# Performance work log

Measured on AMD Instinct MI355X. Metric: run time of the kernel, lower is better.

Reference implementation:

```python
import jax, jax.numpy as jnp
import numpy as np

T, D, H, HD = 2048, 2048, 16, 128
ROPE_BASE = 10000.0
NEG = jnp.float32(-1e30)


def rms_norm(x):
    # F.rms_norm(x, (x.size(-1),)) with default eps = dtype eps
    eps = jnp.finfo(x.dtype).eps
    return x * jax.lax.rsqrt(jnp.mean(x * x, axis=-1, keepdims=True) + eps)


def rotary(x):
    # x: [1, T, H, hd]; half-split rotation as in Rotary.forward
    hd = x.shape[-1]
    inv_freq = (1.0 / ROPE_BASE) ** (jnp.arange(0, hd, 2, dtype=jnp.float32) / hd)
    t = jnp.arange(x.shape[1], dtype=jnp.float32)
    freqs = jnp.outer(t, inv_freq)                      # [T, hd/2]
    cos = jnp.cos(freqs)[None, :, None, :]
    sin = jnp.sin(freqs)[None, :, None, :]
    x1, x2 = jnp.split(x, 2, axis=-1)
    return jnp.concatenate([x1 * cos + x2 * sin, -x1 * sin + x2 * cos], axis=-1)


def setup_inputs() -> dict:
    key = jax.random.key(0)
    ks = jax.random.split(key, 10)
    w = lambda k, shape: jax.random.normal(k, shape, jnp.float32) * 0.02
    return {
        "x":  jax.random.normal(ks[0], (1, T, D), jnp.float32),
        "vi": jax.random.normal(ks[1], (1, T, H, HD), jnp.float32),
        "x0": jax.random.normal(ks[2], (1, T, D), jnp.float32),
        "wq": w(ks[3], (D, D)),
        "wk": w(ks[4], (D, D)),
        "wv": w(ks[5], (D, D)),
        "wo": w(ks[6], (D, D)),
        "lamb": jnp.float32(0.5),
        "lambdas": jnp.array([1.0, 0.0], jnp.float32),
        "w_fc": w(ks[7], (4 * D, D)),
        "w_proj": w(ks[8], (D, 4 * D)),
    }


def reference(x, vi, x0, wq, wk, wv, wo, lamb, lambdas, w_fc, w_proj):
    # Block: residual blend with initial embedding x0
    xb = lambdas[0] * x + lambdas[1] * x0
    xn = rms_norm(xb)

    # --- CausalSelfAttention ---
    q = (xn @ wq.T).reshape(1, T, H, HD)
    k = (xn @ wk.T).reshape(1, T, H, HD)
    v = (xn @ wv.T).reshape(1, T, H, HD)
    v = (1.0 - lamb) * v + lamb * vi                     # value-embedding blend
    q = rotary(rms_norm(q))
    k = rotary(rms_norm(k))

    scale = 1.0 / jnp.sqrt(jnp.float32(HD))              # flex_attention default scale
    scores = jnp.einsum('bqhd,bkhd->bhqk', q, k) * scale # [1,H,T,T]
    causal = jnp.tril(jnp.ones((T, T), bool))
    scores = jnp.where(causal[None, None], scores, NEG)
    attn = jax.nn.softmax(scores, axis=-1)
    y = jnp.einsum('bhqk,bkhd->bqhd', attn, v).reshape(1, T, D)
    a = y @ wo.T                                         # attention output REPLACES x (no residual)

    # --- MLP with squared ReLU ---
    h = rms_norm(a) @ w_fc.T
    h = jnp.square(jax.nn.relu(h))
    out = a + h @ w_proj.T
    return out
```

## Files before the change

### kernel.cpp

```cpp
#include <hip/hip_runtime.h>
#include <hip/hip_bf16.h>

typedef __bf16 bf16;
typedef __bf16 bf16x8 __attribute__((ext_vector_type(8)));
typedef float f32x4 __attribute__((ext_vector_type(4)));
typedef unsigned int u32x4 __attribute__((ext_vector_type(4)));

#define DD 2048
#define DD2 4194304ull
#define G10_LDS 65536

__device__ __forceinline__ void glds16(const void* g, void* l) {
  __builtin_amdgcn_global_load_lds((const __attribute__((address_space(1))) void*)g,
                                   (__attribute__((address_space(3))) void*)l, 16, 0, 0);
}

__device__ __forceinline__ f32x4 mfma16(bf16x8 a, bf16x8 b, f32x4 c) {
  return __builtin_amdgcn_mfma_f32_16x16x32_bf16(a, b, c, 0, 0, 0);
}

__device__ __forceinline__ unsigned pk2(float lo, float hi) {
  unsigned short a = __builtin_bit_cast(unsigned short, (bf16)lo);
  unsigned short b = __builtin_bit_cast(unsigned short, (bf16)hi);
  return (unsigned)a | ((unsigned)b << 16);
}

__global__ __launch_bounds__(256) void cvt_seg(const float* __restrict__ s0, const float* __restrict__ s1,
                                               const float* __restrict__ s2, const float* __restrict__ s3,
                                               bf16* __restrict__ dst, int seglog, size_t total) {
  size_t i = ((size_t)blockIdx.x * 256 + threadIdx.x) * 16;
  const size_t stride = (size_t)gridDim.x * 256 * 16;
  for (; i < total; i += stride) {
    int seg = (int)(i >> seglog);
    const float* src = (seg == 0) ? s0 : (seg == 1) ? s1 : (seg == 2) ? s2 : s3;
    size_t loc = i - ((size_t)seg << seglog);
    float4 a0 = *(const float4*)(src + loc);
    float4 a1 = *(const float4*)(src + loc + 4);
    float4 a2 = *(const float4*)(src + loc + 8);
    float4 a3 = *(const float4*)(src + loc + 12);
    bf16x8 o0, o1;
    o0[0] = (bf16)a0.x; o0[1] = (bf16)a0.y; o0[2] = (bf16)a0.z; o0[3] = (bf16)a0.w;
    o0[4] = (bf16)a1.x; o0[5] = (bf16)a1.y; o0[6] = (bf16)a1.z; o0[7] = (bf16)a1.w;
    o1[0] = (bf16)a2.x; o1[1] = (bf16)a2.y; o1[2] = (bf16)a2.z; o1[3] = (bf16)a2.w;
    o1[4] = (bf16)a3.x; o1[5] = (bf16)a3.y; o1[6] = (bf16)a3.z; o1[7] = (bf16)a3.w;
    *(bf16x8*)(dst + i) = o0;
    *(bf16x8*)(dst + i + 8) = o1;
  }
}

template<bool BLEND>
__global__ __launch_bounds__(256) void prenorm_k(const float* __restrict__ x, const float* __restrict__ x0,
                                                 const float* __restrict__ lambdas, bf16* __restrict__ out) {
  const int t = blockIdx.x, tid = threadIdx.x;
  const float4* xr = (const float4*)(x + (size_t)t * DD);
  float4 a0 = xr[2 * tid], a1 = xr[2 * tid + 1];
  float v[8] = {a0.x, a0.y, a0.z, a0.w, a1.x, a1.y, a1.z, a1.w};
  if (BLEND) {
    const float l0 = lambdas[0], l1 = lambdas[1];
    const float4* yr = (const float4*)(x0 + (size_t)t * DD);
    float4 b0 = yr[2 * tid], b1 = yr[2 * tid + 1];
    float w[8] = {b0.x, b0.y, b0.z, b0.w, b1.x, b1.y, b1.z, b1.w};
#pragma unroll
    for (int i = 0; i < 8; ++i) v[i] = l0 * v[i] + l1 * w[i];
  }
  float ss = 0.f;
#pragma unroll
  for (int i = 0; i < 8; ++i) ss += v[i] * v[i];
#pragma unroll
  for (int off = 1; off < 64; off <<= 1) ss += __shfl_xor(ss, off, 64);
  __shared__ float red[4];
  const int wid = tid >> 6;
  if ((tid & 63) == 0) red[wid] = ss;
  __syncthreads();
  ss = red[0] + red[1] + red[2] + red[3];
  const float sc = rsqrtf(ss * (1.0f / DD) + 1.1920928955078125e-07f);
  bf16x8 o;
#pragma unroll
  for (int i = 0; i < 8; ++i) o[i] = (bf16)(v[i] * sc);
  *(bf16x8*)(out + (size_t)t * DD + tid * 8) = o;
}

__global__ __launch_bounds__(256) void rope_k(bf16* __restrict__ qg, bf16* __restrict__ kg) {
  const int tid = threadIdx.x, lane = tid & 63, wid = tid >> 6;
  const int p = blockIdx.x * 4 + wid;
  bf16* base = ((p >> 15) ? kg : qg);
  const int t = (p >> 4) & 2047, hh = p & 15;
  base += (size_t)t * DD + hh * 128;
  float x1 = (float)base[lane], x2 = (float)base[lane + 64];
  float ss = x1 * x1 + x2 * x2;
#pragma unroll
  for (int off = 1; off < 64; off <<= 1) ss += __shfl_xor(ss, off, 64);
  const float sc = rsqrtf(ss * (1.0f / 128.0f) + 1.1920928955078125e-07f);
  x1 *= sc; x2 *= sc;
  const float fr = (float)t * exp2f((float)lane * (-13.287712379549449f / 64.0f));
  const float s = sinf(fr), c = cosf(fr);
  base[lane]      = (bf16)(x1 * c + x2 * s);
  base[lane + 64] = (bf16)(-x1 * s + x2 * c);
}

__global__ __launch_bounds__(256) void vt_k(const bf16* __restrict__ v, bf16* __restrict__ vt) {
  __shared__ alignas(16) bf16 tile[16 * 128];
  const int tb = blockIdx.x, hb = blockIdx.y, tid = threadIdx.x;
  glds16(v + (size_t)(tb * 16 + (tid >> 4)) * DD + hb * 128 + (tid & 15) * 8, tile + tid * 8);
  __syncthreads();
  const int d_l = tid & 127, tc = tid >> 7;
  bf16x8 o;
#pragma unroll
  for (int i = 0; i < 8; ++i) o[i] = tile[(tc * 8 + i) * 128 + d_l];
  *(bf16x8*)(vt + (size_t)(hb * 128 + d_l) * DD + tb * 16 + tc * 8) = o;
}

__device__ __forceinline__ void g10_stageA(const bf16* A, int Kstride, int row0, int k0,
                                           bf16* buf, int hm, int tid) {
  int prl = tid >> 3, slot = tid & 7;
  int wmb = prl >> 5, r31 = prl & 31;
  glds16(A + (size_t)(row0 + wmb * 64 + hm * 32 + r31) * Kstride + k0 + ((slot ^ (prl & 7)) * 8),
         buf + hm * 4096 + tid * 8);
}
__device__ __forceinline__ void g10_stageB(const bf16* B, int Kstride, int col0, int k0,
                                           bf16* buf, int hn, int tid) {
  int pbl = tid >> 3, slot = tid & 7;
  int wnb = pbl >> 4, c15 = pbl & 15;
  glds16(B + (size_t)(col0 + wnb * 32 + hn * 16 + c15) * Kstride + k0 + ((slot ^ (pbl & 7)) * 8),
         buf + 8192 + hn * 4096 + tid * 8);
}

__device__ __forceinline__ void gemm10_core(const bf16* __restrict__ A, const bf16* __restrict__ B,
                                            int Kstride, int Klen, int row0, int col0,
                                            bf16* smem, f32x4 (&acc)[4][2]) {
  const int tid = threadIdx.x, lane = tid & 63, wid = tid >> 6;
  const int wm = wid >> 2, wn = wid & 3;
  const int l15 = lane & 15, g = lane >> 4;
  const int NT = Klen >> 6;
  g10_stageA(A, Kstride, row0, 0, smem, 0, tid);
  g10_stageB(B, Kstride, col0, 0, smem, 0, tid);
  g10_stageB(B, Kstride, col0, 0, smem, 1, tid);
  g10_stageA(A, Kstride, row0, 0, smem, 1, tid);
  asm volatile("s_waitcnt vmcnt(2)" ::: "memory");
  __builtin_amdgcn_s_barrier();

  bf16x8 a[2][2], b0[2], b1[2];
  for (int t = 0; t < NT; ++t) {
    bf16* cb = smem + (t & 1) * 16384;
    bf16* nb = smem + ((t + 1) & 1) * 16384;
    const int kst = (t + 1) << 6;
    const bool st = (t + 1) < NT;
#pragma unroll
    for (int mm = 0; mm < 2; ++mm)
#pragma unroll
      for (int ks = 0; ks < 2; ++ks) {
        int pr = wm * 32 + mm * 16 + l15;
        a[mm][ks] = *(const bf16x8*)(cb + pr * 64 + (((ks * 4 + g) ^ (pr & 7)) * 8));
      }
#pragma unroll
    for (int ks = 0; ks < 2; ++ks) {
      int pb = wn * 16 + l15;
      b0[ks] = *(const bf16x8*)(cb + 8192 + pb * 64 + (((ks * 4 + g) ^ (pb & 7)) * 8));
    }
    if (st) { g10_stageA(A, Kstride, row0, kst, nb, 0, tid);
              asm volatile("s_waitcnt vmcnt(2)" ::: "memory"); }
    else    { asm volatile("s_waitcnt vmcnt(1)" ::: "memory"); }
    __builtin_amdgcn_s_barrier();
    __builtin_amdgcn_s_setprio(1);
#pragma unroll
    for (int mm = 0; mm < 2; ++mm)
#pragma unroll
      for (int ks = 0; ks < 2; ++ks)
        acc[mm][0] = mfma16(a[mm][ks], b0[ks], acc[mm][0]);
    __builtin_amdgcn_s_setprio(0);
#pragma unroll
    for (int ks = 0; ks < 2; ++ks) {
      int pb = wn * 16 + l15;
      b1[ks] = *(const bf16x8*)(cb + 8192 + 4096 + pb * 64 + (((ks * 4 + g) ^ (pb & 7)) * 8));
    }
    if (st) { g10_stageB(B, Kstride, col0, kst, nb, 0, tid);
              asm volatile("s_waitcnt vmcnt(2)" ::: "memory"); }
    else    { asm volatile("s_waitcnt vmcnt(0)" ::: "memory"); }
    __builtin_amdgcn_s_barrier();
    __builtin_amdgcn_s_setprio(1);
#pragma unroll
    for (int mm = 0; mm < 2; ++mm)
#pragma unroll
      for (int ks = 0; ks < 2; ++ks)
        acc[mm][1] = mfma16(a[mm][ks], b1[ks], acc[mm][1]);
    __builtin_amdgcn_s_setprio(0);
#pragma unroll
    for (int mm = 0; mm < 2; ++mm)
#pragma unroll
      for (int ks = 0; ks < 2; ++ks) {
        int pr = 64 + wm * 32 + mm * 16 + l15;
        a[mm][ks] = *(const bf16x8*)(cb + pr * 64 + (((ks * 4 + g) ^ (pr & 7)) * 8));
      }
    if (st) g10_stageB(B, Kstride, col0, kst, nb, 1, tid);
    __builtin_amdgcn_s_barrier();
    __builtin_amdgcn_s_setprio(1);
#pragma unroll
    for (int mm = 0; mm < 2; ++mm)
#pragma unroll
      for (int ks = 0; ks < 2; ++ks)
        acc[2 + mm][0] = mfma16(a[mm][ks], b0[ks], acc[2 + mm][0]);
    __builtin_amdgcn_s_setprio(0);
    if (st) { g10_stageA(A, Kstride, row0, kst, nb, 1, tid);
              asm volatile("s_waitcnt vmcnt(2)" ::: "memory"); }
    __builtin_amdgcn_s_barrier();
    __builtin_amdgcn_s_setprio(1);
#pragma unroll
    for (int mm = 0; mm < 2; ++mm)
#pragma unroll
      for (int ks = 0; ks < 2; ++ks)
        acc[2 + mm][1] = mfma16(a[mm][ks], b1[ks], acc[2 + mm][1]);
    __builtin_amdgcn_s_setprio(0);
  }
}

#define GEMM10_EPI(STMT)                                                       \
  { const int lane_ = threadIdx.x & 63, wid_ = threadIdx.x >> 6;               \
    const int l15_ = lane_ & 15, g_ = lane_ >> 4;                              \
    const int wm_ = wid_ >> 2, wn_ = wid_ & 3;                                 \
    _Pragma("unroll") for (int m = 0; m < 4; ++m)                              \
    _Pragma("unroll") for (int n = 0; n < 2; ++n)                              \
    _Pragma("unroll") for (int j = 0; j < 4; ++j) {                            \
      int grow = row0 + wm_ * 64 + (m >> 1) * 32 + (m & 1) * 16 + g_ * 4 + j;  \
      int gcol = col0 + wn_ * 32 + n * 16 + l15_;                              \
      float vacc = acc[m][n][j];                                               \
      STMT; } }

__global__ __launch_bounds__(512, 4) void gemm10_qkv(const bf16* __restrict__ A,
    const bf16* __restrict__ Wq, const bf16* __restrict__ Wk, const bf16* __restrict__ Wv,
    bf16* __restrict__ oq, bf16* __restrict__ ok, bf16* __restrict__ ov,
    const float* __restrict__ vi, const float* __restrict__ lambp) {
  extern __shared__ bf16 smem10[];
  const int z = blockIdx.z;
  const bf16* B = (z == 0) ? Wq : (z == 1) ? Wk : Wv;
  bf16* out = (z == 0) ? oq : (z == 1) ? ok : ov;
  const int row0 = blockIdx.y * 128, col0 = blockIdx.x * 128;
  f32x4 acc[4][2] = {};
  gemm10_core(A, B, DD, DD, row0, col0, smem10, acc);
  if (z < 2) {
    GEMM10_EPI( out[(size_t)grow * DD + gcol] = (bf16)vacc; )
  } else {
    const float lam = *lambp;
    GEMM10_EPI( out[(size_t)grow * DD + gcol] =
                  (bf16)((1.0f - lam) * vacc + lam * vi[(size_t)grow * DD + gcol]); )
  }
}

__global__ __launch_bounds__(512, 4) void gemm10_part(const bf16* __restrict__ A, const bf16* __restrict__ B,
                                                      float* __restrict__ o1, int N, int Kstride, int Klen) {
  extern __shared__ bf16 smem10[];
  const int row0 = blockIdx.y * 128, col0 = blockIdx.x * 128;
  const int kofs = blockIdx.z * Klen;
  float* out = o1 + (size_t)blockIdx.z * DD2;
  f32x4 acc[4][2] = {};
  gemm10_core(A + kofs, B + kofs, Kstride, Klen, row0, col0, smem10, acc);
  GEMM10_EPI( out[(size_t)grow * N + gcol] = vacc; )
}

__global__ __launch_bounds__(512, 4) void gemm10_relu(const bf16* __restrict__ A, const bf16* __restrict__ B,
                                                      bf16* __restrict__ out, int N, int Kstride, int Klen) {
  extern __shared__ bf16 smem10[];
  const int row0 = blockIdx.y * 128, col0 = blockIdx.x * 128;
  f32x4 acc[4][2] = {};
  gemm10_core(A, B, Kstride, Klen, row0, col0, smem10, acc);
  GEMM10_EPI( float r = fmaxf(vacc, 0.f); out[(size_t)grow * N + gcol] = (bf16)(r * r); )
}

__global__ __launch_bounds__(256) void wo_red_prenorm(const float* __restrict__ pa,
                                                      float* __restrict__ a_f, bf16* __restrict__ an) {
  const int t = blockIdx.x, tid = threadIdx.x;
  const size_t base = (size_t)t * DD + tid * 8;
  float v[8];
#pragma unroll
  for (int h = 0; h < 2; ++h) {
    size_t i = base + h * 4;
    float4 r0 = *(const float4*)(pa + i);
    float4 r1 = *(const float4*)(pa + DD2 + i);
    v[h*4+0] = r0.x + r1.x;
    v[h*4+1] = r0.y + r1.y;
    v[h*4+2] = r0.z + r1.z;
    v[h*4+3] = r0.w + r1.w;
  }
  *(float4*)(a_f + base)     = make_float4(v[0], v[1], v[2], v[3]);
  *(float4*)(a_f + base + 4) = make_float4(v[4], v[5], v[6], v[7]);
  float ss = 0.f;
#pragma unroll
  for (int i = 0; i < 8; ++i) ss += v[i] * v[i];
#pragma unroll
  for (int off = 1; off < 64; off <<= 1) ss += __shfl_xor(ss, off, 64);
  __shared__ float red[4];
  if ((tid & 63) == 0) red[tid >> 6] = ss;
  __syncthreads();
  ss = red[0] + red[1] + red[2] + red[3];
  const float sc = rsqrtf(ss * (1.0f / DD) + 1.1920928955078125e-07f);
  bf16x8 o;
#pragma unroll
  for (int i = 0; i < 8; ++i) o[i] = (bf16)(v[i] * sc);
  *(bf16x8*)(an + base) = o;
}

__global__ __launch_bounds__(256) void proj_red(const float* __restrict__ pa,
                                                const float* __restrict__ a_f, float* __restrict__ out) {
  const size_t base = ((size_t)blockIdx.x * 256 + threadIdx.x) * 8;
#pragma unroll
  for (int h = 0; h < 2; ++h) {
    size_t i = base + h * 4;
    float4 r = *(const float4*)(a_f + i);
    float4 u = *(const float4*)(pa + i);
    float4 w = *(const float4*)(pa + DD2 + i);
    *(float4*)(out + i) = make_float4(r.x + u.x + w.x, r.y + u.y + w.y,
                                      r.z + u.z + w.z, r.w + u.w + w.w);
  }
}

__device__ __forceinline__ void att_stageK(const bf16* kg, int h, int kt, bf16* dst, int tid) {
#pragma unroll
  for (int r = 0; r < 2; ++r) {
    int e = tid + r * 256, row = e >> 4, slot = e & 15;
    glds16(kg + (size_t)(kt * 32 + row) * DD + h * 128 + ((slot ^ (row & 7)) * 8), dst + e * 8);
  }
}
__device__ __forceinline__ void att_stageV(const bf16* vtg, int h, int kt, bf16* dst, int tid) {
#pragma unroll
  for (int r = 0; r < 2; ++r) {
    int e = tid + r * 256, d = e >> 2, slot = e & 3;
    glds16(vtg + (size_t)(h * 128 + d) * DD + kt * 32 + ((slot ^ ((d >> 1) & 3)) * 8), dst + e * 8);
  }
}

__global__ __launch_bounds__(256) void attn_k(const bf16* __restrict__ qg, const bf16* __restrict__ kg,
                                              const bf16* __restrict__ vtg, bf16* __restrict__ yg) {
  __shared__ alignas(16) bf16 Ks[3][32 * 128];
  __shared__ alignas(16) bf16 Vt[3][128 * 32];
  const int h = blockIdx.y, qb = 31 - blockIdx.x;
  const int tid = threadIdx.x, lane = tid & 63, wid = tid >> 6;
  const int l15 = lane & 15, g = lane >> 4, swl = l15 & 7;
  const int qrow = qb * 64 + wid * 16;
  const float scale = 0.08838834764831845f;
  bf16x8 aQ[4];
  {
    const bf16* qp = qg + (size_t)(qrow + l15) * DD + h * 128 + g * 8;
#pragma unroll
    for (int kc = 0; kc < 4; ++kc) aQ[kc] = *(const bf16x8*)(qp + kc * 32);
  }
  f32x4 acc[8] = {};
  float lsum = 0.f;
  const int nkt = qb * 2 + 2;
  att_stageK(kg, h, 0, Ks[0], tid);
  att_stageV(vtg, h, 0, Vt[0], tid);
  att_stageK(kg, h, 1, Ks[1], tid);
  att_stageV(vtg, h, 1, Vt[1], tid);
  asm volatile("s_waitcnt vmcnt(4)" ::: "memory");
  __builtin_amdgcn_s_barrier();
  int cur = 0;
  for (int kt = 0; kt < nkt; ++kt) {
    const int kbase = kt * 32;
    const int nb = (cur >= 1) ? cur - 1 : 2;
    bf16x8 kf0[4], kf1[4];
#pragma unroll
    for (int kc = 0; kc < 4; ++kc) {
      kf0[kc] = *(const bf16x8*)(Ks[cur] + l15 * 128 + (((kc * 4 + g) ^ swl) * 8));
      kf1[kc] = *(const bf16x8*)(Ks[cur] + (16 + l15) * 128 + (((kc * 4 + g) ^ swl) * 8));
    }
    if (kt + 2 < nkt) { att_stageK(kg, h, kt + 2, Ks[nb], tid);
                        att_stageV(vtg, h, kt + 2, Vt[nb], tid); }
    f32x4 S0 = {}, S1 = {};
#pragma unroll
    for (int kc = 0; kc < 4; ++kc) {
      S0 = mfma16(kf0[kc], aQ[kc], S0);
      S1 = mfma16(kf1[kc], aQ[kc], S1);
    }
    const int q = qrow + l15;
    float p0[4], p1[4];
#pragma unroll
    for (int j = 0; j < 4; ++j) {
      int k0 = kbase + 4 * g + j;
      p0[j] = (k0 <= q) ? __expf(S0[j] * scale) : 0.f;
      p1[j] = (k0 + 16 <= q) ? __expf(S1[j] * scale) : 0.f;
      lsum += p0[j] + p1[j];
    }
    unsigned w0 = pk2(p0[0], p0[1]), w1 = pk2(p0[2], p0[3]);
    unsigned w2 = pk2(p1[0], p1[1]), w3 = pk2(p1[2], p1[3]);
    const int s0l = (g & 1) * 32 + l15, s1l = s0l + 16;
    const bool hi = g >= 2;
    unsigned t00 = __shfl(w0, s0l, 64), t10 = __shfl(w1, s0l, 64);
    unsigned t01 = __shfl(w0, s1l, 64), t11 = __shfl(w1, s1l, 64);
    unsigned u00 = __shfl(w2, s0l, 64), u10 = __shfl(w3, s0l, 64);
    unsigned u01 = __shfl(w2, s1l, 64), u11 = __shfl(w3, s1l, 64);
    u32x4 av = { hi ? u00 : t00, hi ? u10 : t10, hi ? u01 : t01, hi ? u11 : t11 };
    bf16x8 aP = __builtin_bit_cast(bf16x8, av);
#pragma unroll
    for (int dt = 0; dt < 8; ++dt) {
      int d = dt * 16 + l15;
      bf16x8 bV = *(const bf16x8*)(Vt[cur] + d * 32 + ((g ^ ((d >> 1) & 3)) * 8));
      acc[dt] = mfma16(aP, bV, acc[dt]);
    }
    if (kt + 1 < nkt) {
      if (kt + 2 < nkt) { asm volatile("s_waitcnt vmcnt(4)" ::: "memory"); }
      else              { asm volatile("s_waitcnt vmcnt(0)" ::: "memory"); }
      __builtin_amdgcn_s_barrier();
    }
    cur = (cur == 2) ? 0 : cur + 1;
  }
  lsum += __shfl_xor(lsum, 16, 64);
  lsum += __shfl_xor(lsum, 32, 64);
  f32x4 linv;
#pragma unroll
  for (int j = 0; j < 4; ++j) linv[j] = 1.0f / __shfl(lsum, 4 * g + j, 64);
#pragma unroll
  for (int dt = 0; dt < 8; ++dt)
#pragma unroll
    for (int j = 0; j < 4; ++j) {
      int q = qrow + 4 * g + j;
      yg[(size_t)q * DD + h * 128 + dt * 16 + l15] = (bf16)(acc[dt][j] * linv[j]);
    }
}

extern "C" void kernel_launch(void* const* d_in, const int* in_sizes, int n_in,
                              void* d_out, int out_size, void* d_ws, size_t ws_size,
                              hipStream_t stream) {
  const float* x       = (const float*)d_in[0];
  const float* vi      = (const float*)d_in[1];
  const float* x0      = (const float*)d_in[2];
  const float* wq      = (const float*)d_in[3];
  const float* wk      = (const float*)d_in[4];
  const float* wv      = (const float*)d_in[5];
  const float* wo      = (const float*)d_in[6];
  const float* lamb    = (const float*)d_in[7];
  const float* lambdas = (const float*)d_in[8];
  const float* wfc     = (const float*)d_in[9];
  const float* wproj   = (const float*)d_in[10];
  float* out = (float*)d_out;

  (void)hipFuncSetAttribute(reinterpret_cast<const void*>(gemm10_qkv),
                            hipFuncAttributeMaxDynamicSharedMemorySize, G10_LDS);
  (void)hipFuncSetAttribute(reinterpret_cast<const void*>(gemm10_part),
                            hipFuncAttributeMaxDynamicSharedMemorySize, G10_LDS);
  (void)hipFuncSetAttribute(reinterpret_cast<const void*>(gemm10_relu),
                            hipFuncAttributeMaxDynamicSharedMemorySize, G10_LDS);

  char* wsb = (char*)d_ws;
  size_t off = 0;
  auto alloc = [&](size_t bytes) { void* p = wsb + off; off = (off + bytes + 255) & ~(size_t)255; return p; };
  bf16* wq_b  = (bf16*)alloc(DD2 * 2);
  bf16* wk_b  = (bf16*)alloc(DD2 * 2);
  bf16* wv_b  = (bf16*)alloc(DD2 * 2);
  bf16* wo_b  = (bf16*)alloc(DD2 * 2);
  bf16* wfc_b = (bf16*)alloc(DD2 * 8);
  bf16* wpj_b = (bf16*)alloc(DD2 * 8);
  bf16* xn_b  = (bf16*)alloc(DD2 * 2);
  bf16* q_b   = (bf16*)alloc(DD2 * 2);
  bf16* k_b   = (bf16*)alloc(DD2 * 2);
  bf16* v_b   = (bf16*)alloc(DD2 * 2);
  bf16* y_b   = (bf16*)alloc(DD2 * 2);
  bf16* an_b  = (bf16*)alloc(DD2 * 2);
  float* partA = (float*)xn_b;
  float* a_f  = (float*)alloc(DD2 * 4);
  bf16* h_b   = (bf16*)alloc(DD2 * 8);
  bf16* vt_b  = h_b;

  cvt_seg<<<2048, 256, 0, stream>>>(wq, wk, wv, wo, (bf16*)wsb, 22, 4 * DD2);
  prenorm_k<true><<<2048, 256, 0, stream>>>(x, x0, lambdas, xn_b);
  gemm10_qkv<<<dim3(16, 16, 3), 512, G10_LDS, stream>>>(xn_b, wq_b, wk_b, wv_b, q_b, k_b, v_b, vi, lamb);
  rope_k<<<16384, 256, 0, stream>>>(q_b, k_b);
  vt_k<<<dim3(128, 16), 256, 0, stream>>>(v_b, vt_b);
  attn_k<<<dim3(32, 16), 256, 0, stream>>>(q_b, k_b, vt_b, y_b);
  gemm10_part<<<dim3(16, 16, 2), 512, G10_LDS, stream>>>(y_b, wo_b, partA, DD, DD, 1024);
  wo_red_prenorm<<<2048, 256, 0, stream>>>(partA, a_f, an_b);
  cvt_seg<<<2048, 256, 0, stream>>>(wfc, wproj, wfc, wfc, wfc_b, 24, 8 * DD2);
  gemm10_relu<<<dim3(64, 16), 512, G10_LDS, stream>>>(an_b, wfc_b, h_b, 4 * DD, DD, DD);
  gemm10_part<<<dim3(16, 16, 2), 512, G10_LDS, stream>>>(h_b, wpj_b, partA, DD, 4 * DD, 4096);
  proj_red<<<2048, 256, 0, stream>>>(partA, a_f, out);
}
```

Baseline: 387.5 us.

## Use 256x256-tile GEMM for QKV and FC projections, swizzle block order

Adds a new GEMM core with 256x256 output tiles per 512-thread block (8x4 MFMA accumulators per wave, 128KB LDS double-buffered) and uses it for the QKV and FC+ReLU² GEMMs in place of the 128x128 kernel. The larger tiles raise arithmetic intensity and cut global/L2 traffic per FLOP. The cost is occupancy of one block per CU and fewer blocks: 192 for QKV and 256 for FC, which may underfill the 256 CUs. A grouped block-index swizzle is also added to the split-K partial GEMM and the new FC kernel to improve L2 locality.

Result: no change. 381.2 us (-1.6%).

```diff
diff --git a/kernel.cpp b/kernel.cpp
--- a/kernel.cpp
+++ b/kernel.cpp
@@ -8,6 +8,7 @@
 
 #define DD 2048
 #define DD2 4194304ull
+#define G9_LDS 131072
 #define G10_LDS 65536
 
 __device__ __forceinline__ void glds16(const void* g, void* l) {
@@ -110,6 +111,166 @@
   *(bf16x8*)(vt + (size_t)(hb * 128 + d_l) * DD + tb * 16 + tc * 8) = o;
 }
 
+__device__ __forceinline__ void g9_stageA(const bf16* A, int Kstride, int row0, int k0,
+                                          bf16* buf, int hm, int tid) {
+#pragma unroll
+  for (int i = 0; i < 2; ++i) {
+    int e = tid + i * 512;
+    int prl = e >> 3, slot = e & 7;
+    int wm = prl >> 6, r63 = prl & 63;
+    glds16(A + (size_t)(row0 + wm * 128 + hm * 64 + r63) * Kstride + k0 + ((slot ^ (prl & 7)) * 8),
+           buf + hm * 8192 + e * 8);
+  }
+}
+__device__ __forceinline__ void g9_stageB(const bf16* B, int Kstride, int col0, int k0,
+                                          bf16* buf, int hn, int tid) {
+#pragma unroll
+  for (int i = 0; i < 2; ++i) {
+    int e = tid + i * 512;
+    int pbl = e >> 3, slot = e & 7;
+    int wn = pbl >> 5, q = pbl & 31;
+    glds16(B + (size_t)(col0 + wn * 64 + hn * 32 + q) * Kstride + k0 + ((slot ^ (pbl & 7)) * 8),
+           buf + 16384 + hn * 8192 + e * 8);
+  }
+}
+
+__device__ __forceinline__ void gemm9_core(const bf16* __restrict__ A, const bf16* __restrict__ B,
+                                           int Kstride, int Klen, int row0, int col0,
+                                           bf16* smem, f32x4 (&acc)[8][4]) {
+  const int tid = threadIdx.x, lane = tid & 63, wid = tid >> 6;
+  const int wm = wid >> 2, wn = wid & 3;
+  const int l15 = lane & 15, g = lane >> 4;
+  const int sw = l15 & 7;
+  const int NT = Klen >> 6;
+  g9_stageA(A, Kstride, row0, 0, smem, 0, tid);
+  g9_stageB(B, Kstride, col0, 0, smem, 0, tid);
+  g9_stageB(B, Kstride, col0, 0, smem, 1, tid);
+  g9_stageA(A, Kstride, row0, 0, smem, 1, tid);
+  g9_stageA(A, Kstride, row0, 64, smem + 32768, 0, tid);
+  g9_stageB(B, Kstride, col0, 64, smem + 32768, 0, tid);
+  asm volatile("s_waitcnt vmcnt(8)" ::: "memory");
+  __builtin_amdgcn_s_barrier();
+
+  bf16x8 a[4][2], b0[2][2], b1[2][2];
+  for (int t = 0; t < NT; ++t) {
+    bf16* cb = smem + (t & 1) * 32768;
+    bf16* nb = smem + ((t + 1) & 1) * 32768;
+    const bool s1 = (t + 1) < NT, s2 = (t + 2) < NT;
+#pragma unroll
+    for (int mm = 0; mm < 4; ++mm)
+#pragma unroll
+      for (int ks = 0; ks < 2; ++ks)
+        a[mm][ks] = *(const bf16x8*)(cb + (wm * 64 + mm * 16 + l15) * 64 + (((ks * 4 + g) ^ sw) * 8));
+#pragma unroll
+    for (int nn = 0; nn < 2; ++nn)
+#pragma unroll
+      for (int ks = 0; ks < 2; ++ks)
+        b0[nn][ks] = *(const bf16x8*)(cb + 16384 + (wn * 32 + nn * 16 + l15) * 64 + (((ks * 4 + g) ^ sw) * 8));
+    if (s1) { g9_stageB(B, Kstride, col0, (t + 1) << 6, nb, 1, tid);
+              g9_stageA(A, Kstride, row0, (t + 1) << 6, nb, 1, tid);
+              asm volatile("s_waitcnt vmcnt(8)" ::: "memory"); }
+    else    { asm volatile("s_waitcnt vmcnt(0)" ::: "memory"); }
+    __builtin_amdgcn_s_barrier();
+    __builtin_amdgcn_s_setprio(1);
+#pragma unroll
+    for (int mm = 0; mm < 4; ++mm)
+#pragma unroll
+      for (int nn = 0; nn < 2; ++nn)
+#pragma unroll
+        for (int ks = 0; ks < 2; ++ks)
+          acc[mm][nn] = mfma16(a[mm][ks], b0[nn][ks], acc[mm][nn]);
+    __builtin_amdgcn_s_setprio(0);
+#pragma unroll
+    for (int nn = 0; nn < 2; ++nn)
+#pragma unroll
+      for (int ks = 0; ks < 2; ++ks)
+        b1[nn][ks] = *(const bf16x8*)(cb + 16384 + 8192 + (wn * 32 + nn * 16 + l15) * 64 + (((ks * 4 + g) ^ sw) * 8));
+    __builtin_amdgcn_s_barrier();
+    __builtin_amdgcn_s_setprio(1);
+#pragma unroll
+    for (int mm = 0; mm < 4; ++mm)
+#pragma unroll
+      for (int nn = 0; nn < 2; ++nn)
+#pragma unroll
+        for (int ks = 0; ks < 2; ++ks)
+          acc[mm][2 + nn] = mfma16(a[mm][ks], b1[nn][ks], acc[mm][2 + nn]);
+    __builtin_amdgcn_s_setprio(0);
+#pragma unroll
+    for (int mm = 0; mm < 4; ++mm)
+#pragma unroll
+      for (int ks = 0; ks < 2; ++ks)
+        a[mm][ks] = *(const bf16x8*)(cb + 8192 + (wm * 64 + mm * 16 + l15) * 64 + (((ks * 4 + g) ^ sw) * 8));
+    __builtin_amdgcn_s_barrier();
+    __builtin_amdgcn_s_setprio(1);
+#pragma unroll
+    for (int mm = 0; mm < 4; ++mm)
+#pragma unroll
+      for (int nn = 0; nn < 2; ++nn)
+#pragma unroll
+        for (int ks = 0; ks < 2; ++ks)
+          acc[4 + mm][nn] = mfma16(a[mm][ks], b0[nn][ks], acc[4 + mm][nn]);
+    __builtin_amdgcn_s_setprio(0);
+    if (s2) { g9_stageA(A, Kstride, row0, (t + 2) << 6, cb, 0, tid);
+              g9_stageB(B, Kstride, col0, (t + 2) << 6, cb, 0, tid);
+              asm volatile("s_waitcnt vmcnt(8)" ::: "memory"); }
+    else if (s1) { asm volatile("s_waitcnt vmcnt(4)" ::: "memory"); }
+    __builtin_amdgcn_s_barrier();
+    __builtin_amdgcn_s_setprio(1);
+#pragma unroll
+    for (int mm = 0; mm < 4; ++mm)
+#pragma unroll
+      for (int nn = 0; nn < 2; ++nn)
+#pragma unroll
+        for (int ks = 0; ks < 2; ++ks)
+          acc[4 + mm][2 + nn] = mfma16(a[mm][ks], b1[nn][ks], acc[4 + mm][2 + nn]);
+    __builtin_amdgcn_s_setprio(0);
+  }
+}
+
+#define GEMM9_EPI(STMT)                                                        \
+  { const int lane_ = threadIdx.x & 63, wid_ = threadIdx.x >> 6;               \
+    const int l15_ = lane_ & 15, g_ = lane_ >> 4;                              \
+    const int wm_ = wid_ >> 2, wn_ = wid_ & 3;                                 \
+    _Pragma("unroll") for (int m = 0; m < 8; ++m)                              \
+    _Pragma("unroll") for (int n = 0; n < 4; ++n)                              \
+    _Pragma("unroll") for (int j = 0; j < 4; ++j) {                            \
+      int grow = row0 + wm_ * 128 + (m >> 2) * 64 + (m & 3) * 16 + g_ * 4 + j; \
+      int gcol = col0 + wn_ * 64 + (n >> 1) * 32 + (n & 1) * 16 + l15_;        \
+      float vacc = acc[m][n][j];                                               \
+      STMT; } }
+
+__global__ __launch_bounds__(512, 1) void gemm9_qkv(const bf16* __restrict__ A,
+    const bf16* __restrict__ Wq, const bf16* __restrict__ Wk, const bf16* __restrict__ Wv,
+    bf16* __restrict__ oq, bf16* __restrict__ ok, bf16* __restrict__ ov,
+    const float* __restrict__ vi, const float* __restrict__ lambp) {
+  extern __shared__ bf16 smem9[];
+  const int z = blockIdx.z;
+  const bf16* B = (z == 0) ? Wq : (z == 1) ? Wk : Wv;
+  bf16* out = (z == 0) ? oq : (z == 1) ? ok : ov;
+  const int row0 = blockIdx.y * 256, col0 = blockIdx.x * 256;
+  f32x4 acc[8][4] = {};
+  gemm9_core(A, B, DD, DD, row0, col0, smem9, acc);
+  if (z < 2) {
+    GEMM9_EPI( out[(size_t)grow * DD + gcol] = (bf16)vacc; )
+  } else {
+    const float lam = *lambp;
+    GEMM9_EPI( out[(size_t)grow * DD + gcol] =
+                 (bf16)((1.0f - lam) * vacc + lam * vi[(size_t)grow * DD + gcol]); )
+  }
+}
+
+__global__ __launch_bounds__(512, 1) void gemm9_relu(const bf16* __restrict__ A, const bf16* __restrict__ B,
+                                                     bf16* __restrict__ out, int N, int Kstride, int Klen) {
+  extern __shared__ bf16 smem9[];
+  const int nb = gridDim.x * gridDim.y;
+  const int lid = blockIdx.y * gridDim.x + blockIdx.x;
+  const int swz = (lid & 7) * (nb >> 3) + (lid >> 3);
+  const int row0 = (swz / gridDim.x) * 256, col0 = (swz % gridDim.x) * 256;
+  f32x4 acc[8][4] = {};
+  gemm9_core(A, B, Kstride, Klen, row0, col0, smem9, acc);
+  GEMM9_EPI( float r = fmaxf(vacc, 0.f); out[(size_t)grow * N + gcol] = (bf16)(r * r); )
+}
+
 __device__ __forceinline__ void g10_stageA(const bf16* A, int Kstride, int row0, int k0,
                                            bf16* buf, int hm, int tid) {
   int prl = tid >> 3, slot = tid & 7;
@@ -225,44 +386,18 @@
       float vacc = acc[m][n][j];                                               \
       STMT; } }
 
-__global__ __launch_bounds__(512, 4) void gemm10_qkv(const bf16* __restrict__ A,
-    const bf16* __restrict__ Wq, const bf16* __restrict__ Wk, const bf16* __restrict__ Wv,
-    bf16* __restrict__ oq, bf16* __restrict__ ok, bf16* __restrict__ ov,
-    const float* __restrict__ vi, const float* __restrict__ lambp) {
-  extern __shared__ bf16 smem10[];
-  const int z = blockIdx.z;
-  const bf16* B = (z == 0) ? Wq : (z == 1) ? Wk : Wv;
-  bf16* out = (z == 0) ? oq : (z == 1) ? ok : ov;
-  const int row0 = blockIdx.y * 128, col0 = blockIdx.x * 128;
-  f32x4 acc[4][2] = {};
-  gemm10_core(A, B, DD, DD, row0, col0, smem10, acc);
-  if (z < 2) {
-    GEMM10_EPI( out[(size_t)grow * DD + gcol] = (bf16)vacc; )
-  } else {
-    const float lam = *lambp;
-    GEMM10_EPI( out[(size_t)grow * DD + gcol] =
-                  (bf16)((1.0f - lam) * vacc + lam * vi[(size_t)grow * DD + gcol]); )
-  }
-}
-
 __global__ __launch_bounds__(512, 4) void gemm10_part(const bf16* __restrict__ A, const bf16* __restrict__ B,
                                                       float* __restrict__ o1, int N, int Kstride, int Klen) {
   extern __shared__ bf16 smem10[];
-  const int row0 = blockIdx.y * 128, col0 = blockIdx.x * 128;
+  const int nb = gridDim.x * gridDim.y;
+  const int lid = blockIdx.y * gridDim.x + blockIdx.x;
+  const int swz = (lid & 7) * (nb >> 3) + (lid >> 3);
+  const int row0 = (swz / gridDim.x) * 128, col0 = (swz % gridDim.x) * 128;
   const int kofs = blockIdx.z * Klen;
   float* out = o1 + (size_t)blockIdx.z * DD2;
   f32x4 acc[4][2] = {};
   gemm10_core(A + kofs, B + kofs, Kstride, Klen, row0, col0, smem10, acc);
   GEMM10_EPI( out[(size_t)grow * N + gcol] = vacc; )
-}
-
-__global__ __launch_bounds__(512, 4) void gemm10_relu(const bf16* __restrict__ A, const bf16* __restrict__ B,
-                                                      bf16* __restrict__ out, int N, int Kstride, int Klen) {
-  extern __shared__ bf16 smem10[];
-  const int row0 = blockIdx.y * 128, col0 = blockIdx.x * 128;
-  f32x4 acc[4][2] = {};
-  gemm10_core(A, B, Kstride, Klen, row0, col0, smem10, acc);
-  GEMM10_EPI( float r = fmaxf(vacc, 0.f); out[(size_t)grow * N + gcol] = (bf16)(r * r); )
 }
 
 __global__ __launch_bounds__(256) void wo_red_prenorm(const float* __restrict__ pa,
@@ -431,11 +566,11 @@
   const float* wproj   = (const float*)d_in[10];
   float* out = (float*)d_out;
 
-  (void)hipFuncSetAttribute(reinterpret_cast<const void*>(gemm10_qkv),
-                            hipFuncAttributeMaxDynamicSharedMemorySize, G10_LDS);
+  (void)hipFuncSetAttribute(reinterpret_cast<const void*>(gemm9_qkv),
+                            hipFuncAttributeMaxDynamicSharedMemorySize, G9_LDS);
+  (void)hipFuncSetAttribute(reinterpret_cast<const void*>(gemm9_relu),
+                            hipFuncAttributeMaxDynamicSharedMemorySize, G9_LDS);
   (void)hipFuncSetAttribute(reinterpret_cast<const void*>(gemm10_part),
-                            hipFuncAttributeMaxDynamicSharedMemorySize, G10_LDS);
-  (void)hipFuncSetAttribute(reinterpret_cast<const void*>(gemm10_relu),
                             hipFuncAttributeMaxDynamicSharedMemorySize, G10_LDS);
 
   char* wsb = (char*)d_ws;
@@ -460,14 +595,14 @@
 
   cvt_seg<<<2048, 256, 0, stream>>>(wq, wk, wv, wo, (bf16*)wsb, 22, 4 * DD2);
   prenorm_k<true><<<2048, 256, 0, stream>>>(x, x0, lambdas, xn_b);
-  gemm10_qkv<<<dim3(16, 16, 3), 512, G10_LDS, stream>>>(xn_b, wq_b, wk_b, wv_b, q_b, k_b, v_b, vi, lamb);
+  gemm9_qkv<<<dim3(8, 8, 3), 512, G9_LDS, stream>>>(xn_b, wq_b, wk_b, wv_b, q_b, k_b, v_b, vi, lamb);
   rope_k<<<16384, 256, 0, stream>>>(q_b, k_b);
   vt_k<<<dim3(128, 16), 256, 0, stream>>>(v_b, vt_b);
   attn_k<<<dim3(32, 16), 256, 0, stream>>>(q_b, k_b, vt_b, y_b);
   gemm10_part<<<dim3(16, 16, 2), 512, G10_LDS, stream>>>(y_b, wo_b, partA, DD, DD, 1024);
   wo_red_prenorm<<<2048, 256, 0, stream>>>(partA, a_f, an_b);
   cvt_seg<<<2048, 256, 0, stream>>>(wfc, wproj, wfc, wfc, wfc_b, 24, 8 * DD2);
-  gemm10_relu<<<dim3(64, 16), 512, G10_LDS, stream>>>(an_b, wfc_b, h_b, 4 * DD, DD, DD);
+  gemm9_relu<<<dim3(32, 8), 512, G9_LDS, stream>>>(an_b, wfc_b, h_b, 4 * DD, DD, DD);
   gemm10_part<<<dim3(16, 16, 2), 512, G10_LDS, stream>>>(h_b, wpj_b, partA, DD, 4 * DD, 4096);
   proj_red<<<2048, 256, 0, stream>>>(partA, a_f, out);
 }
```
